# Optimization experiments

Measured on AMD Instinct MI355X. Metric: run time of the kernel, lower is better.

The kernel has to match this reference:

```python
import jax, jax.numpy as jnp
import numpy as np

ATOM_FDIM = 35
BOND_FDIM = 5
MAX_NB = 15
HIDDEN = 512
DEPTH = 6
N_MOLS = 1024
ATOMS_PER_MOL = 32
N_ATOMS = N_MOLS * ATOMS_PER_MOL      # 32768
N_BONDS = 2 * N_ATOMS                  # 65536 (each bond appears in both directions)
N_MESS = 8192                          # tree messages (row 0 is the zero pad slot)
TOTAL_MSG = N_MESS + N_BONDS           # index space for agraph/bgraph


def setup_inputs() -> dict:
    key = jax.random.key(0)
    ks = jax.random.split(key, 8)
    fatoms = jax.random.normal(ks[0], (N_ATOMS, ATOM_FDIM), jnp.float32)
    fbonds = jax.random.normal(ks[1], (N_BONDS, ATOM_FDIM + BOND_FDIM), jnp.float32)
    agraph = jax.random.randint(ks[2], (N_ATOMS, MAX_NB), 0, TOTAL_MSG, dtype=jnp.int32)
    bgraph = jax.random.randint(ks[3], (N_BONDS, MAX_NB), 0, TOTAL_MSG, dtype=jnp.int32)
    # row 0 of the concatenated message table is the padding slot -> zero it
    tree_message = jax.random.normal(ks[4], (N_MESS, HIDDEN), jnp.float32).at[0].set(0.0)
    starts = jnp.arange(N_MOLS, dtype=jnp.int32) * ATOMS_PER_MOL
    scope = jnp.stack([starts, jnp.full((N_MOLS,), ATOMS_PER_MOL, jnp.int32)], axis=1)
    s_i = 1.0 / np.sqrt(ATOM_FDIM + BOND_FDIM)
    s_h = 1.0 / np.sqrt(HIDDEN)
    s_o = 1.0 / np.sqrt(ATOM_FDIM + HIDDEN)
    W_i = jax.random.normal(ks[5], (ATOM_FDIM + BOND_FDIM, HIDDEN), jnp.float32) * s_i
    W_h = jax.random.normal(ks[6], (HIDDEN, HIDDEN), jnp.float32) * s_h
    W_o = jax.random.normal(ks[7], (ATOM_FDIM + HIDDEN, HIDDEN), jnp.float32) * s_o
    b_o = jnp.zeros((HIDDEN,), jnp.float32)
    return {"fatoms": fatoms, "fbonds": fbonds, "agraph": agraph, "bgraph": bgraph,
            "scope": scope, "tree_message": tree_message,
            "W_i": W_i, "W_h": W_h, "W_o": W_o, "b_o": b_o}


def reference(fatoms, fbonds, agraph, bgraph, scope, tree_message, W_i, W_h, W_o, b_o):
    binput = fbonds @ W_i                         # [B, H]
    graph_message = jax.nn.relu(binput)

    def step(gm, _):
        message = jnp.concatenate([tree_message, gm], axis=0)   # [M+B, H]
        nei = message[bgraph].sum(axis=1)                       # gather-sum [B, H]
        return jax.nn.relu(binput + nei @ W_h), None

    graph_message, _ = jax.lax.scan(step, graph_message, None, length=DEPTH - 1)

    message = jnp.concatenate([tree_message, graph_message], axis=0)
    nei = message[agraph].sum(axis=1)             # [A, H]
    ainput = jnp.concatenate([fatoms, nei], axis=1)
    atom_hiddens = jax.nn.relu(ainput @ W_o + b_o)

    # scope is uniform (st = i*ATOMS_PER_MOL, le = ATOMS_PER_MOL) -> static segment ids
    seg = jnp.repeat(jnp.arange(N_MOLS), ATOMS_PER_MOL)
    sums = jax.ops.segment_sum(atom_hiddens, seg, num_segments=N_MOLS)
    return sums / scope[:, 1:].astype(atom_hiddens.dtype)
```

## Files before the change

kernel.cpp:

```cpp
#include <hip/hip_runtime.h>
#include <stdint.h>


#define MAX_NB 15
#define HID 512
#define NA 32768
#define NB 65536
#define NMESS 8192

typedef unsigned short u16;
typedef unsigned int u32;
typedef __bf16 bf16x8 __attribute__((ext_vector_type(8)));
typedef float f32x4 __attribute__((ext_vector_type(4)));

__device__ __forceinline__ u16 f2bf(float f) {
  u32 u = __builtin_bit_cast(u32, f);
  u32 r = (u + 0x7fffu + ((u >> 16) & 1u)) >> 16;
  return (u16)r;
}
__device__ __forceinline__ float bf2f(u16 b) {
  u32 u = ((u32)b) << 16;
  return __builtin_bit_cast(float, u);
}
__device__ __forceinline__ float bflo(u32 u) {
  return __builtin_bit_cast(float, u << 16);
}
__device__ __forceinline__ float bfhi(u32 u) {
  return __builtin_bit_cast(float, u & 0xffff0000u);
}

__device__ __forceinline__ void async16(const u16* g, u16* l) {
  __builtin_amdgcn_global_load_lds(
      (const __attribute__((address_space(1))) u32*)g,
      (__attribute__((address_space(3))) u32*)l, 16, 0, 0);
}

__global__ __launch_bounds__(256) void prep_kernel(
    const float* __restrict__ fbonds, const float* __restrict__ tree,
    const float* __restrict__ Wi, const float* __restrict__ Wh,
    const float* __restrict__ Wo, u16* __restrict__ msg,
    u16* __restrict__ fbpad, u16* __restrict__ wi_t, u16* __restrict__ wh_t,
    u16* __restrict__ wo_t) {
  int t = blockIdx.x * 256 + threadIdx.x;
  const int N0 = NMESS * HID;
  const int N1 = NB * 64;
  const int N2 = 512 * 64;
  const int N3 = 512 * 512;
  const int N4 = 512 * 576;
  if (t < N0) { msg[t] = f2bf(tree[t]); return; }
  t -= N0;
  if (t < N1) {
    int row = t >> 6, c = t & 63;
    fbpad[t] = (c < 40) ? f2bf(fbonds[row * 40 + c]) : (u16)0;
    return;
  }
  t -= N1;
  if (t < N2) {
    int n = t >> 6, k = t & 63;
    wi_t[t] = (k < 40) ? f2bf(Wi[k * 512 + n]) : (u16)0;
    return;
  }
  t -= N2;
  if (t < N3) {
    int n = t >> 9, k = t & 511;
    wh_t[t] = f2bf(Wh[k * 512 + n]);
    return;
  }
  t -= N3;
  if (t < N4) {
    int n = t / 576, k = t - n * 576;
    float v = 0.f;
    if (k < 512) v = Wo[(35 + k) * 512 + n];
    else if (k < 547) v = Wo[(k - 512) * 512 + n];
    wo_t[t] = f2bf(v);
    return;
  }
}

__global__ __launch_bounds__(256) void gather_bonds(
    const u16* __restrict__ msg, const int* __restrict__ bgraph,
    u16* __restrict__ nei) {
  const int xcd = blockIdx.x & 7;
  const int chunk = blockIdx.x >> 3;
  int row = xcd * (NB / 8) + chunk * 4 + (threadIdx.x >> 6);
  int lane = threadIdx.x & 63;
  const int* idxp = bgraph + row * MAX_NB;
  float acc[8] = {0, 0, 0, 0, 0, 0, 0, 0};
#pragma unroll
  for (int j = 0; j < MAX_NB; j++) {
    int id = idxp[j];
    uint4 v = *(const uint4*)(msg + (size_t)id * HID + lane * 8);
    acc[0] += bflo(v.x); acc[1] += bfhi(v.x);
    acc[2] += bflo(v.y); acc[3] += bfhi(v.y);
    acc[4] += bflo(v.z); acc[5] += bfhi(v.z);
    acc[6] += bflo(v.w); acc[7] += bfhi(v.w);
  }
  uint4 o;
  o.x = (u32)f2bf(acc[0]) | ((u32)f2bf(acc[1]) << 16);
  o.y = (u32)f2bf(acc[2]) | ((u32)f2bf(acc[3]) << 16);
  o.z = (u32)f2bf(acc[4]) | ((u32)f2bf(acc[5]) << 16);
  o.w = (u32)f2bf(acc[6]) | ((u32)f2bf(acc[7]) << 16);
  *(uint4*)(nei + (size_t)row * HID + lane * 8) = o;
}

__global__ __launch_bounds__(256) void gather_atoms(
    const u16* __restrict__ msg, const int* __restrict__ agraph,
    const float* __restrict__ fatoms, u16* __restrict__ ainput) {
  const int xcd = blockIdx.x & 7;
  const int chunk = blockIdx.x >> 3;
  int row = xcd * (NA / 8) + chunk * 4 + (threadIdx.x >> 6);
  int lane = threadIdx.x & 63;
  const int* idxp = agraph + row * MAX_NB;
  float acc[8] = {0, 0, 0, 0, 0, 0, 0, 0};
#pragma unroll
  for (int j = 0; j < MAX_NB; j++) {
    int id = idxp[j];
    uint4 v = *(const uint4*)(msg + (size_t)id * HID + lane * 8);
    acc[0] += bflo(v.x); acc[1] += bfhi(v.x);
    acc[2] += bflo(v.y); acc[3] += bfhi(v.y);
    acc[4] += bflo(v.z); acc[5] += bfhi(v.z);
    acc[6] += bflo(v.w); acc[7] += bfhi(v.w);
  }
  uint4 o;
  o.x = (u32)f2bf(acc[0]) | ((u32)f2bf(acc[1]) << 16);
  o.y = (u32)f2bf(acc[2]) | ((u32)f2bf(acc[3]) << 16);
  o.z = (u32)f2bf(acc[4]) | ((u32)f2bf(acc[5]) << 16);
  o.w = (u32)f2bf(acc[6]) | ((u32)f2bf(acc[7]) << 16);
  u16* arow = ainput + (size_t)row * 576;
  *(uint4*)(arow + lane * 8) = o;
  float tv = (lane < 35) ? fatoms[(size_t)row * 35 + lane] : 0.f;
  arow[512 + lane] = f2bf(tv);
}

template <int EPI>
__global__ __launch_bounds__(256) void gemm_k(
    const u16* __restrict__ A, const u16* __restrict__ Bt, int K, int mtx,
    u16* __restrict__ binput, u16* __restrict__ msgout,
    const float* __restrict__ bo, const int* __restrict__ scope,
    float* __restrict__ out) {
  __shared__ __align__(16) u16 As[128 * 32];
  __shared__ __align__(16) u16 Bs[128 * 32];
  const int L = blockIdx.x;
  const int xcd = L & 7;
  const int q = L >> 3;
  const int mBase = (xcd * mtx + (q >> 2)) * 128;
  const int nBase = (q & 3) * 128;
  const int t = threadIdx.x;
  const int lane = t & 63;
  const int w = t >> 6;
  const int wm = w & 1, wn = w >> 1;
  const int r = t >> 2;
  const int c8 = (t & 3) * 8;
  const int q8 = (lane >> 4) * 8;
  const int l15 = lane & 15;

  f32x4 acc[4][4];
#pragma unroll
  for (int i = 0; i < 4; i++)
#pragma unroll
    for (int j = 0; j < 4; j++)
#pragma unroll
      for (int rg = 0; rg < 4; rg++) acc[i][j][rg] = 0.f;

  for (int kb = 0; kb < K; kb += 32) {
    __syncthreads();
    async16(A + (size_t)(mBase + r) * K + kb + c8, As + r * 32 + c8);
    async16(A + (size_t)(mBase + r + 64) * K + kb + c8, As + (r + 64) * 32 + c8);
    async16(Bt + (size_t)(nBase + r) * K + kb + c8, Bs + r * 32 + c8);
    async16(Bt + (size_t)(nBase + r + 64) * K + kb + c8, Bs + (r + 64) * 32 + c8);
    __syncthreads();
    bf16x8 av[4], bv[4];
#pragma unroll
    for (int i = 0; i < 4; i++)
      av[i] = *(const bf16x8*)(As + (wm * 64 + i * 16 + l15) * 32 + q8);
#pragma unroll
    for (int j = 0; j < 4; j++)
      bv[j] = *(const bf16x8*)(Bs + (wn * 64 + j * 16 + l15) * 32 + q8);
#pragma unroll
    for (int i = 0; i < 4; i++)
#pragma unroll
      for (int j = 0; j < 4; j++)
        acc[i][j] = __builtin_amdgcn_mfma_f32_16x16x32_bf16(av[i], bv[j],
                                                            acc[i][j], 0, 0, 0);
  }

  if (EPI == 2) {
#pragma unroll
    for (int m = 0; m < 2; m++) {
      int mol = (mBase + wm * 64 + m * 32) >> 5;
      float inv_le = 1.0f / (float)scope[mol * 2 + 1];
#pragma unroll
      for (int j = 0; j < 4; j++) {
        int col = nBase + wn * 64 + j * 16 + l15;
        float bias = bo[col];
        float s = 0.f;
#pragma unroll
        for (int i = 2 * m; i < 2 * m + 2; i++)
#pragma unroll
          for (int rg = 0; rg < 4; rg++)
            s += fmaxf(acc[i][j][rg] + bias, 0.f);
        s += __shfl_xor(s, 16, 64);
        s += __shfl_xor(s, 32, 64);
        if (lane < 16) out[(size_t)mol * HID + col] = s * inv_le;
      }
    }
  } else {
#pragma unroll
    for (int i = 0; i < 4; i++) {
      int row = mBase + wm * 64 + i * 16 + (lane >> 4) * 4;
#pragma unroll
      for (int j = 0; j < 4; j++) {
        int col = nBase + wn * 64 + j * 16 + l15;
#pragma unroll
        for (int rg = 0; rg < 4; rg++) {
          float v = acc[i][j][rg];
          size_t gi = (size_t)(row + rg) * HID + col;
          if (EPI == 0) {
            binput[gi] = f2bf(v);
            msgout[gi + (size_t)NMESS * HID] = f2bf(fmaxf(v, 0.f));
          } else {
            v += bf2f(binput[gi]);
            msgout[gi + (size_t)NMESS * HID] = f2bf(fmaxf(v, 0.f));
          }
        }
      }
    }
  }
}

extern "C" void kernel_launch(void* const* d_in, const int* in_sizes, int n_in,
                              void* d_out, int out_size, void* d_ws,
                              size_t ws_size, hipStream_t stream) {
  const float* fatoms = (const float*)d_in[0];
  const float* fbonds = (const float*)d_in[1];
  const int* agraph = (const int*)d_in[2];
  const int* bgraph = (const int*)d_in[3];
  const int* scope = (const int*)d_in[4];
  const float* tree = (const float*)d_in[5];
  const float* Wi = (const float*)d_in[6];
  const float* Wh = (const float*)d_in[7];
  const float* Wo = (const float*)d_in[8];
  const float* bo = (const float*)d_in[9];
  float* out = (float*)d_out;

  char* ws = (char*)d_ws;
  u16* msg = (u16*)(ws);
  u16* binput = (u16*)(ws + 75497472ull);
  u16* nei = (u16*)(ws + 142606336ull);
  u16* wi_t = (u16*)(ws + 209715200ull);
  u16* wh_t = (u16*)(ws + 209780736ull);
  u16* wo_t = (u16*)(ws + 210305024ull);
  u16* fbpad = nei;
  u16* ainput = binput;

  prep_kernel<<<35072, 256, 0, stream>>>(fbonds, tree, Wi, Wh, Wo, msg, fbpad,
                                         wi_t, wh_t, wo_t);

  gemm_k<0><<<2048, 256, 0, stream>>>(fbpad, wi_t, 64, 64, binput, msg,
                                      nullptr, nullptr, nullptr);
  for (int d = 0; d < 5; d++) {
    gather_bonds<<<NB / 4, 256, 0, stream>>>(msg, bgraph, nei);
    gemm_k<1><<<2048, 256, 0, stream>>>(nei, wh_t, 512, 64, binput, msg,
                                        nullptr, nullptr, nullptr);
  }
  gather_atoms<<<NA / 4, 256, 0, stream>>>(msg, agraph, fatoms, ainput);
  gemm_k<2><<<1024, 256, 0, stream>>>(ainput, wo_t, 576, 32, nullptr, nullptr,
                                      bo, scope, out);
}
```

Baseline: 1.257 ms.

## Partition gather by column slices per XCD for L2 locality of message table

Restructures the bond and atom gather kernels so each XCD handles two 32-column slices of the hidden dimension across all rows, instead of whole rows for a subset of rows. The intent is that each XCD's L2 only needs to hold its own column slice of the message table. Indices are staged in shared memory with nontemporal loads, and outputs use nontemporal stores. The trade-off is that each gathered load is now only 16 bytes per lane-group (64B per row slice), which reduces coalescing per row and repeats the index fetch for every slice.

Measured after the change: 1.674 ms. +33.1%, slower.

```diff
diff --git a/kernel.cpp b/kernel.cpp
--- a/kernel.cpp
+++ b/kernel.cpp
@@ -12,6 +12,7 @@
 typedef unsigned int u32;
 typedef __bf16 bf16x8 __attribute__((ext_vector_type(8)));
 typedef float f32x4 __attribute__((ext_vector_type(4)));
+typedef u32 u32x4 __attribute__((ext_vector_type(4)));
 
 __device__ __forceinline__ u16 f2bf(float f) {
   u32 u = __builtin_bit_cast(u32, f);
@@ -80,56 +81,105 @@
 __global__ __launch_bounds__(256) void gather_bonds(
     const u16* __restrict__ msg, const int* __restrict__ bgraph,
     u16* __restrict__ nei) {
-  const int xcd = blockIdx.x & 7;
-  const int chunk = blockIdx.x >> 3;
-  int row = xcd * (NB / 8) + chunk * 4 + (threadIdx.x >> 6);
-  int lane = threadIdx.x & 63;
-  const int* idxp = bgraph + row * MAX_NB;
+  __shared__ int sidx[64 * MAX_NB];
+  const int L = blockIdx.x;
+  const int xcd = L & 7;
+  const int q = L >> 3;
+  const int slice = 2 * xcd + (q >> 10);
+  const int chunk = q & 1023;
+  const int t = threadIdx.x;
+
+  const int* gb = bgraph + chunk * (64 * MAX_NB);
+  for (int i = t; i < 64 * MAX_NB; i += 256)
+    sidx[i] = __builtin_nontemporal_load(gb + i);
+  __syncthreads();
+
+  const int lane = t & 63;
+  const int w = t >> 6;
+  const int rl = w * 16 + (lane >> 2);
+  const int sub = lane & 3;
+  const int row = chunk * 64 + rl;
+  const int colOff = slice * 32 + sub * 8;
+
+  int ids[MAX_NB];
+#pragma unroll
+  for (int j = 0; j < MAX_NB; j++) ids[j] = sidx[rl * MAX_NB + j];
+
   float acc[8] = {0, 0, 0, 0, 0, 0, 0, 0};
 #pragma unroll
   for (int j = 0; j < MAX_NB; j++) {
-    int id = idxp[j];
-    uint4 v = *(const uint4*)(msg + (size_t)id * HID + lane * 8);
+    uint4 v = *(const uint4*)(msg + (size_t)ids[j] * HID + colOff);
     acc[0] += bflo(v.x); acc[1] += bfhi(v.x);
     acc[2] += bflo(v.y); acc[3] += bfhi(v.y);
     acc[4] += bflo(v.z); acc[5] += bfhi(v.z);
     acc[6] += bflo(v.w); acc[7] += bfhi(v.w);
   }
-  uint4 o;
+  u32x4 o;
   o.x = (u32)f2bf(acc[0]) | ((u32)f2bf(acc[1]) << 16);
   o.y = (u32)f2bf(acc[2]) | ((u32)f2bf(acc[3]) << 16);
   o.z = (u32)f2bf(acc[4]) | ((u32)f2bf(acc[5]) << 16);
   o.w = (u32)f2bf(acc[6]) | ((u32)f2bf(acc[7]) << 16);
-  *(uint4*)(nei + (size_t)row * HID + lane * 8) = o;
+  __builtin_nontemporal_store(o, (u32x4*)(nei + (size_t)row * HID + colOff));
 }
 
 __global__ __launch_bounds__(256) void gather_atoms(
     const u16* __restrict__ msg, const int* __restrict__ agraph,
     const float* __restrict__ fatoms, u16* __restrict__ ainput) {
-  const int xcd = blockIdx.x & 7;
-  const int chunk = blockIdx.x >> 3;
-  int row = xcd * (NA / 8) + chunk * 4 + (threadIdx.x >> 6);
-  int lane = threadIdx.x & 63;
-  const int* idxp = agraph + row * MAX_NB;
+  __shared__ int sidx[64 * MAX_NB];
+  const int L = blockIdx.x;
+  const int xcd = L & 7;
+  const int q = L >> 3;
+  const int sl = q >> 9;
+  const int slice = 2 * xcd + sl;
+  const int chunk = q & 511;
+  const int t = threadIdx.x;
+
+  const int* ga = agraph + chunk * (64 * MAX_NB);
+  for (int i = t; i < 64 * MAX_NB; i += 256)
+    sidx[i] = __builtin_nontemporal_load(ga + i);
+  __syncthreads();
+
+  const int lane = t & 63;
+  const int w = t >> 6;
+  const int rl = w * 16 + (lane >> 2);
+  const int sub = lane & 3;
+  const int row = chunk * 64 + rl;
+  const int colOff = slice * 32 + sub * 8;
+
+  int ids[MAX_NB];
+#pragma unroll
+  for (int j = 0; j < MAX_NB; j++) ids[j] = sidx[rl * MAX_NB + j];
+
   float acc[8] = {0, 0, 0, 0, 0, 0, 0, 0};
 #pragma unroll
   for (int j = 0; j < MAX_NB; j++) {
-    int id = idxp[j];
-    uint4 v = *(const uint4*)(msg + (size_t)id * HID + lane * 8);
+    uint4 v = *(const uint4*)(msg + (size_t)ids[j] * HID + colOff);
     acc[0] += bflo(v.x); acc[1] += bfhi(v.x);
     acc[2] += bflo(v.y); acc[3] += bfhi(v.y);
     acc[4] += bflo(v.z); acc[5] += bfhi(v.z);
     acc[6] += bflo(v.w); acc[7] += bfhi(v.w);
   }
-  uint4 o;
+  u16* arow = ainput + (size_t)row * 576;
+  u32x4 o;
   o.x = (u32)f2bf(acc[0]) | ((u32)f2bf(acc[1]) << 16);
   o.y = (u32)f2bf(acc[2]) | ((u32)f2bf(acc[3]) << 16);
   o.z = (u32)f2bf(acc[4]) | ((u32)f2bf(acc[5]) << 16);
   o.w = (u32)f2bf(acc[6]) | ((u32)f2bf(acc[7]) << 16);
-  u16* arow = ainput + (size_t)row * 576;
-  *(uint4*)(arow + lane * 8) = o;
-  float tv = (lane < 35) ? fatoms[(size_t)row * 35 + lane] : 0.f;
-  arow[512 + lane] = f2bf(tv);
+  __builtin_nontemporal_store(o, (u32x4*)(arow + colOff));
+
+  if (xcd == 0 && sl == 0) {
+    u32 tw[8];
+#pragma unroll
+    for (int c = 0; c < 8; c++) {
+      int c0 = sub * 16 + 2 * c;
+      float a = (c0 < 35) ? fatoms[(size_t)row * 35 + c0] : 0.f;
+      float b = (c0 + 1 < 35) ? fatoms[(size_t)row * 35 + c0 + 1] : 0.f;
+      tw[c] = (u32)f2bf(a) | ((u32)f2bf(b) << 16);
+    }
+    uint4* tp = (uint4*)(arow + 512 + sub * 16);
+    tp[0] = make_uint4(tw[0], tw[1], tw[2], tw[3]);
+    tp[1] = make_uint4(tw[4], tw[5], tw[6], tw[7]);
+  }
 }
 
 template <int EPI>
@@ -259,11 +309,11 @@
   gemm_k<0><<<2048, 256, 0, stream>>>(fbpad, wi_t, 64, 64, binput, msg,
                                       nullptr, nullptr, nullptr);
   for (int d = 0; d < 5; d++) {
-    gather_bonds<<<NB / 4, 256, 0, stream>>>(msg, bgraph, nei);
+    gather_bonds<<<16384, 256, 0, stream>>>(msg, bgraph, nei);
     gemm_k<1><<<2048, 256, 0, stream>>>(nei, wh_t, 512, 64, binput, msg,
                                         nullptr, nullptr, nullptr);
   }
-  gather_atoms<<<NA / 4, 256, 0, stream>>>(msg, agraph, fatoms, ainput);
+  gather_atoms<<<8192, 256, 0, stream>>>(msg, agraph, fatoms, ainput);
   gemm_k<2><<<1024, 256, 0, stream>>>(ainput, wo_t, 576, 32, nullptr, nullptr,
                                       bo, scope, out);
 }
```

## Fuse neighbor gather-sum into the W_h/W_o GEMMs with ping-pong message buffers

Applied to the files above, without the earlier changes.

Replaces the separate gather kernels and the nei/ainput intermediates with a fused kernel. Each 32-row block gathers the neighbor sums straight into LDS and then multiplies by B, which it reads directly from global memory without staging. The graph messages now alternate between two buffers, and an offset gap lets the gather address the tree table and the current graph buffer as one index space. This removes one global write and read of the 64 MB intermediate per depth step and halves the launch count, but B is re-read from global by every block and the GEMM tile is smaller.

After: 1.513 ms. +20.3%, slower.

```diff
diff --git a/kernel.cpp b/kernel.cpp
--- a/kernel.cpp
+++ b/kernel.cpp
@@ -7,6 +7,7 @@
 #define NA 32768
 #define NB 65536
 #define NMESS 8192
+#define GAPE 33554432u
 
 typedef unsigned short u16;
 typedef unsigned int u32;
@@ -38,7 +39,7 @@
 __global__ __launch_bounds__(256) void prep_kernel(
     const float* __restrict__ fbonds, const float* __restrict__ tree,
     const float* __restrict__ Wi, const float* __restrict__ Wh,
-    const float* __restrict__ Wo, u16* __restrict__ msg,
+    const float* __restrict__ Wo, u16* __restrict__ tab,
     u16* __restrict__ fbpad, u16* __restrict__ wi_t, u16* __restrict__ wh_t,
     u16* __restrict__ wo_t) {
   int t = blockIdx.x * 256 + threadIdx.x;
@@ -47,7 +48,7 @@
   const int N2 = 512 * 64;
   const int N3 = 512 * 512;
   const int N4 = 512 * 576;
-  if (t < N0) { msg[t] = f2bf(tree[t]); return; }
+  if (t < N0) { tab[t] = f2bf(tree[t]); return; }
   t -= N0;
   if (t < N1) {
     int row = t >> 6, c = t & 63;
@@ -77,73 +78,16 @@
   }
 }
 
-__global__ __launch_bounds__(256) void gather_bonds(
-    const u16* __restrict__ msg, const int* __restrict__ bgraph,
-    u16* __restrict__ nei) {
-  const int xcd = blockIdx.x & 7;
-  const int chunk = blockIdx.x >> 3;
-  int row = xcd * (NB / 8) + chunk * 4 + (threadIdx.x >> 6);
-  int lane = threadIdx.x & 63;
-  const int* idxp = bgraph + row * MAX_NB;
-  float acc[8] = {0, 0, 0, 0, 0, 0, 0, 0};
-#pragma unroll
-  for (int j = 0; j < MAX_NB; j++) {
-    int id = idxp[j];
-    uint4 v = *(const uint4*)(msg + (size_t)id * HID + lane * 8);
-    acc[0] += bflo(v.x); acc[1] += bfhi(v.x);
-    acc[2] += bflo(v.y); acc[3] += bfhi(v.y);
-    acc[4] += bflo(v.z); acc[5] += bfhi(v.z);
-    acc[6] += bflo(v.w); acc[7] += bfhi(v.w);
-  }
-  uint4 o;
-  o.x = (u32)f2bf(acc[0]) | ((u32)f2bf(acc[1]) << 16);
-  o.y = (u32)f2bf(acc[2]) | ((u32)f2bf(acc[3]) << 16);
-  o.z = (u32)f2bf(acc[4]) | ((u32)f2bf(acc[5]) << 16);
-  o.w = (u32)f2bf(acc[6]) | ((u32)f2bf(acc[7]) << 16);
-  *(uint4*)(nei + (size_t)row * HID + lane * 8) = o;
-}
-
-__global__ __launch_bounds__(256) void gather_atoms(
-    const u16* __restrict__ msg, const int* __restrict__ agraph,
-    const float* __restrict__ fatoms, u16* __restrict__ ainput) {
-  const int xcd = blockIdx.x & 7;
-  const int chunk = blockIdx.x >> 3;
-  int row = xcd * (NA / 8) + chunk * 4 + (threadIdx.x >> 6);
-  int lane = threadIdx.x & 63;
-  const int* idxp = agraph + row * MAX_NB;
-  float acc[8] = {0, 0, 0, 0, 0, 0, 0, 0};
-#pragma unroll
-  for (int j = 0; j < MAX_NB; j++) {
-    int id = idxp[j];
-    uint4 v = *(const uint4*)(msg + (size_t)id * HID + lane * 8);
-    acc[0] += bflo(v.x); acc[1] += bfhi(v.x);
-    acc[2] += bflo(v.y); acc[3] += bfhi(v.y);
-    acc[4] += bflo(v.z); acc[5] += bfhi(v.z);
-    acc[6] += bflo(v.w); acc[7] += bfhi(v.w);
-  }
-  uint4 o;
-  o.x = (u32)f2bf(acc[0]) | ((u32)f2bf(acc[1]) << 16);
-  o.y = (u32)f2bf(acc[2]) | ((u32)f2bf(acc[3]) << 16);
-  o.z = (u32)f2bf(acc[4]) | ((u32)f2bf(acc[5]) << 16);
-  o.w = (u32)f2bf(acc[6]) | ((u32)f2bf(acc[7]) << 16);
-  u16* arow = ainput + (size_t)row * 576;
-  *(uint4*)(arow + lane * 8) = o;
-  float tv = (lane < 35) ? fatoms[(size_t)row * 35 + lane] : 0.f;
-  arow[512 + lane] = f2bf(tv);
-}
-
-template <int EPI>
-__global__ __launch_bounds__(256) void gemm_k(
-    const u16* __restrict__ A, const u16* __restrict__ Bt, int K, int mtx,
-    u16* __restrict__ binput, u16* __restrict__ msgout,
-    const float* __restrict__ bo, const int* __restrict__ scope,
-    float* __restrict__ out) {
+__global__ __launch_bounds__(256) void gemm_init(
+    const u16* __restrict__ A, const u16* __restrict__ Bt,
+    u16* __restrict__ binput, u16* __restrict__ graphA) {
+  const int K = 64;
   __shared__ __align__(16) u16 As[128 * 32];
   __shared__ __align__(16) u16 Bs[128 * 32];
   const int L = blockIdx.x;
   const int xcd = L & 7;
   const int q = L >> 3;
-  const int mBase = (xcd * mtx + (q >> 2)) * 128;
+  const int mBase = (xcd * 64 + (q >> 2)) * 128;
   const int nBase = (q & 3) * 128;
   const int t = threadIdx.x;
   const int lane = t & 63;
@@ -184,44 +128,136 @@
                                                             acc[i][j], 0, 0, 0);
   }
 
-  if (EPI == 2) {
-#pragma unroll
-    for (int m = 0; m < 2; m++) {
-      int mol = (mBase + wm * 64 + m * 32) >> 5;
-      float inv_le = 1.0f / (float)scope[mol * 2 + 1];
-#pragma unroll
-      for (int j = 0; j < 4; j++) {
-        int col = nBase + wn * 64 + j * 16 + l15;
-        float bias = bo[col];
-        float s = 0.f;
-#pragma unroll
-        for (int i = 2 * m; i < 2 * m + 2; i++)
-#pragma unroll
-          for (int rg = 0; rg < 4; rg++)
-            s += fmaxf(acc[i][j][rg] + bias, 0.f);
-        s += __shfl_xor(s, 16, 64);
-        s += __shfl_xor(s, 32, 64);
-        if (lane < 16) out[(size_t)mol * HID + col] = s * inv_le;
+#pragma unroll
+  for (int i = 0; i < 4; i++) {
+    int row = mBase + wm * 64 + i * 16 + (lane >> 4) * 4;
+#pragma unroll
+    for (int j = 0; j < 4; j++) {
+      int col = nBase + wn * 64 + j * 16 + l15;
+#pragma unroll
+      for (int rg = 0; rg < 4; rg++) {
+        float v = acc[i][j][rg];
+        size_t gi = (size_t)(row + rg) * HID + col;
+        binput[gi] = f2bf(v);
+        graphA[gi] = f2bf(fmaxf(v, 0.f));
       }
     }
+  }
+}
+
+template <int ATOMS>
+__global__ __launch_bounds__(256, 3) void fused_gg(
+    const u16* __restrict__ tab, const int* __restrict__ graph,
+    const u16* __restrict__ Bt, const u16* __restrict__ binput,
+    const float* __restrict__ fatoms, const float* __restrict__ bo,
+    const int* __restrict__ scope, u16* __restrict__ outGraph,
+    float* __restrict__ out, u32 gap) {
+  constexpr int K = ATOMS ? 576 : 512;
+  constexpr int NT = K / 32;
+  __shared__ __align__(16) u16 As[NT * 1024];
+  __shared__ int sidx[32 * MAX_NB];
+  const int mBase = blockIdx.x * 32;
+  const int t = threadIdx.x;
+  for (int i = t; i < 32 * MAX_NB; i += 256)
+    sidx[i] = graph[mBase * MAX_NB + i];
+  __syncthreads();
+
+  const int lane = t & 63;
+  const int w = t >> 6;
+  for (int r = 0; r < 8; r++) {
+    const int rl = w * 8 + r;
+    float acc[8] = {0, 0, 0, 0, 0, 0, 0, 0};
+#pragma unroll
+    for (int j = 0; j < MAX_NB; j++) {
+      int id = sidx[rl * MAX_NB + j];
+      u32 off = (u32)id * HID + (id >= NMESS ? gap : 0u);
+      uint4 v = *(const uint4*)(tab + off + lane * 8);
+      acc[0] += bflo(v.x); acc[1] += bfhi(v.x);
+      acc[2] += bflo(v.y); acc[3] += bfhi(v.y);
+      acc[4] += bflo(v.z); acc[5] += bfhi(v.z);
+      acc[6] += bflo(v.w); acc[7] += bfhi(v.w);
+    }
+    uint4 o;
+    o.x = (u32)f2bf(acc[0]) | ((u32)f2bf(acc[1]) << 16);
+    o.y = (u32)f2bf(acc[2]) | ((u32)f2bf(acc[3]) << 16);
+    o.z = (u32)f2bf(acc[4]) | ((u32)f2bf(acc[5]) << 16);
+    o.w = (u32)f2bf(acc[6]) | ((u32)f2bf(acc[7]) << 16);
+    *(uint4*)(As + (lane >> 2) * 1024 + rl * 32 + (lane & 3) * 8) = o;
+    if (ATOMS) {
+      if (lane < 8) {
+        u32 tw[4];
+#pragma unroll
+        for (int c = 0; c < 4; c++) {
+          int c0 = lane * 8 + 2 * c;
+          float a = (c0 < 35) ? fatoms[(size_t)(mBase + rl) * 35 + c0] : 0.f;
+          float b =
+              (c0 + 1 < 35) ? fatoms[(size_t)(mBase + rl) * 35 + c0 + 1] : 0.f;
+          tw[c] = (u32)f2bf(a) | ((u32)f2bf(b) << 16);
+        }
+        *(uint4*)(As + (16 + (lane >> 2)) * 1024 + rl * 32 + (lane & 3) * 8) =
+            make_uint4(tw[0], tw[1], tw[2], tw[3]);
+      }
+    }
+  }
+  __syncthreads();
+
+  const int l15 = lane & 15;
+  const int q8 = (lane >> 4) * 8;
+  const int nq = w;
+  f32x4 acc2[2][8];
+#pragma unroll
+  for (int i = 0; i < 2; i++)
+#pragma unroll
+    for (int j = 0; j < 8; j++)
+#pragma unroll
+      for (int rg = 0; rg < 4; rg++) acc2[i][j][rg] = 0.f;
+
+  for (int kbi = 0; kbi < NT; kbi++) {
+    bf16x8 av0 = *(const bf16x8*)(As + kbi * 1024 + l15 * 32 + q8);
+    bf16x8 av1 = *(const bf16x8*)(As + kbi * 1024 + (16 + l15) * 32 + q8);
+    bf16x8 bv[8];
+#pragma unroll
+    for (int j = 0; j < 8; j++)
+      bv[j] = *(const bf16x8*)(Bt + (size_t)(nq * 128 + j * 16 + l15) * K +
+                               kbi * 32 + q8);
+#pragma unroll
+    for (int j = 0; j < 8; j++) {
+      acc2[0][j] =
+          __builtin_amdgcn_mfma_f32_16x16x32_bf16(av0, bv[j], acc2[0][j], 0, 0, 0);
+      acc2[1][j] =
+          __builtin_amdgcn_mfma_f32_16x16x32_bf16(av1, bv[j], acc2[1][j], 0, 0, 0);
+    }
+  }
+
+  if (ATOMS) {
+    const int mol = blockIdx.x;
+    float inv = 1.0f / (float)scope[mol * 2 + 1];
+#pragma unroll
+    for (int j = 0; j < 8; j++) {
+      int col = nq * 128 + j * 16 + l15;
+      float bias = bo[col];
+      float s = 0.f;
+#pragma unroll
+      for (int i = 0; i < 2; i++)
+#pragma unroll
+        for (int rg = 0; rg < 4; rg++)
+          s += fmaxf(acc2[i][j][rg] + bias, 0.f);
+      s += __shfl_xor(s, 16, 64);
+      s += __shfl_xor(s, 32, 64);
+      if (lane < 16) out[(size_t)mol * HID + col] = s * inv;
+    }
   } else {
 #pragma unroll
-    for (int i = 0; i < 4; i++) {
-      int row = mBase + wm * 64 + i * 16 + (lane >> 4) * 4;
-#pragma unroll
-      for (int j = 0; j < 4; j++) {
-        int col = nBase + wn * 64 + j * 16 + l15;
+    for (int i = 0; i < 2; i++) {
+      int row = mBase + i * 16 + (lane >> 4) * 4;
+#pragma unroll
+      for (int j = 0; j < 8; j++) {
+        int col = nq * 128 + j * 16 + l15;
 #pragma unroll
         for (int rg = 0; rg < 4; rg++) {
-          float v = acc[i][j][rg];
           size_t gi = (size_t)(row + rg) * HID + col;
-          if (EPI == 0) {
-            binput[gi] = f2bf(v);
-            msgout[gi + (size_t)NMESS * HID] = f2bf(fmaxf(v, 0.f));
-          } else {
-            v += bf2f(binput[gi]);
-            msgout[gi + (size_t)NMESS * HID] = f2bf(fmaxf(v, 0.f));
-          }
+          float v = acc2[i][j][rg] + bf2f(binput[gi]);
+          outGraph[gi] = f2bf(fmaxf(v, 0.f));
         }
       }
     }
@@ -243,27 +279,27 @@
   const float* bo = (const float*)d_in[9];
   float* out = (float*)d_out;
 
-  char* ws = (char*)d_ws;
-  u16* msg = (u16*)(ws);
-  u16* binput = (u16*)(ws + 75497472ull);
-  u16* nei = (u16*)(ws + 142606336ull);
-  u16* wi_t = (u16*)(ws + 209715200ull);
-  u16* wh_t = (u16*)(ws + 209780736ull);
-  u16* wo_t = (u16*)(ws + 210305024ull);
-  u16* fbpad = nei;
-  u16* ainput = binput;
-
-  prep_kernel<<<35072, 256, 0, stream>>>(fbonds, tree, Wi, Wh, Wo, msg, fbpad,
+  u16* tab = (u16*)d_ws;
+  u16* graphA = tab + (size_t)NMESS * HID;
+  u16* graphB = graphA + (size_t)NB * HID;
+  u16* binput = graphB + (size_t)NB * HID;
+  u16* wi_t = binput + (size_t)NB * HID;
+  u16* wh_t = wi_t + 512 * 64;
+  u16* wo_t = wh_t + 512 * 512;
+  u16* fbpad = graphB;
+
+  prep_kernel<<<35072, 256, 0, stream>>>(fbonds, tree, Wi, Wh, Wo, tab, fbpad,
                                          wi_t, wh_t, wo_t);
 
-  gemm_k<0><<<2048, 256, 0, stream>>>(fbpad, wi_t, 64, 64, binput, msg,
-                                      nullptr, nullptr, nullptr);
+  gemm_init<<<2048, 256, 0, stream>>>(fbpad, wi_t, binput, graphA);
+
+  const u32 gaps[5] = {0u, GAPE, 0u, GAPE, 0u};
+  u16* const outs[5] = {graphB, graphA, graphB, graphA, graphB};
   for (int d = 0; d < 5; d++) {
-    gather_bonds<<<NB / 4, 256, 0, stream>>>(msg, bgraph, nei);
-    gemm_k<1><<<2048, 256, 0, stream>>>(nei, wh_t, 512, 64, binput, msg,
-                                        nullptr, nullptr, nullptr);
-  }
-  gather_atoms<<<NA / 4, 256, 0, stream>>>(msg, agraph, fatoms, ainput);
-  gemm_k<2><<<1024, 256, 0, stream>>>(ainput, wo_t, 576, 32, nullptr, nullptr,
-                                      bo, scope, out);
-}
+    fused_gg<0><<<2048, 256, 0, stream>>>(tab, bgraph, wh_t, binput, nullptr,
+                                          nullptr, nullptr, outs[d], nullptr,
+                                          gaps[d]);
+  }
+  fused_gg<1><<<1024, 256, 0, stream>>>(tab, agraph, wo_t, nullptr, fatoms, bo,
+                                        scope, nullptr, out, GAPE);
+}
```

## Recompute bond input inside depth GEMM by concatenating W_i and W_h along K

Applied to the files above, without the earlier changes.

Instead of storing binput (fbonds@W_i) and reloading it in every depth-step epilogue, each depth GEMM now runs over a concatenated K dimension: the padded fbonds (64 cols) followed by the gathered neighbor sum (512 cols), against a stacked W_i/W_h weight matrix. This removes the binput write and the five bf16 binput reads of a 65536x512 matrix, and it also avoids rounding binput to bf16. In exchange each depth GEMM does about 12% more MFMA work and the K loop picks its source pointer per iteration.

Result: no change. 1.243 ms (-1.1%).

```diff
diff --git a/kernel.cpp b/kernel.cpp
--- a/kernel.cpp
+++ b/kernel.cpp
@@ -18,10 +18,6 @@
   u32 r = (u + 0x7fffu + ((u >> 16) & 1u)) >> 16;
   return (u16)r;
 }
-__device__ __forceinline__ float bf2f(u16 b) {
-  u32 u = ((u32)b) << 16;
-  return __builtin_bit_cast(float, u);
-}
 __device__ __forceinline__ float bflo(u32 u) {
   return __builtin_bit_cast(float, u << 16);
 }
@@ -39,14 +35,12 @@
     const float* __restrict__ fbonds, const float* __restrict__ tree,
     const float* __restrict__ Wi, const float* __restrict__ Wh,
     const float* __restrict__ Wo, u16* __restrict__ msg,
-    u16* __restrict__ fbpad, u16* __restrict__ wi_t, u16* __restrict__ wh_t,
-    u16* __restrict__ wo_t) {
+    u16* __restrict__ fbpad, u16* __restrict__ wcat, u16* __restrict__ wo_t) {
   int t = blockIdx.x * 256 + threadIdx.x;
   const int N0 = NMESS * HID;
   const int N1 = NB * 64;
-  const int N2 = 512 * 64;
-  const int N3 = 512 * 512;
-  const int N4 = 512 * 576;
+  const int N2 = 512 * 576;
+  const int N3 = 512 * 576;
   if (t < N0) { msg[t] = f2bf(tree[t]); return; }
   t -= N0;
   if (t < N1) {
@@ -56,18 +50,15 @@
   }
   t -= N1;
   if (t < N2) {
-    int n = t >> 6, k = t & 63;
-    wi_t[t] = (k < 40) ? f2bf(Wi[k * 512 + n]) : (u16)0;
+    int n = t / 576, k = t - n * 576;
+    float v = 0.f;
+    if (k < 40) v = Wi[k * 512 + n];
+    else if (k >= 64) v = Wh[(k - 64) * 512 + n];
+    wcat[t] = f2bf(v);
     return;
   }
   t -= N2;
   if (t < N3) {
-    int n = t >> 9, k = t & 511;
-    wh_t[t] = f2bf(Wh[k * 512 + n]);
-    return;
-  }
-  t -= N3;
-  if (t < N4) {
     int n = t / 576, k = t - n * 576;
     float v = 0.f;
     if (k < 512) v = Wo[(35 + k) * 512 + n];
@@ -134,10 +125,10 @@
 
 template <int EPI>
 __global__ __launch_bounds__(256) void gemm_k(
-    const u16* __restrict__ A, const u16* __restrict__ Bt, int K, int mtx,
-    u16* __restrict__ binput, u16* __restrict__ msgout,
-    const float* __restrict__ bo, const int* __restrict__ scope,
-    float* __restrict__ out) {
+    const u16* __restrict__ A1, int s1, int kSplit,
+    const u16* __restrict__ A2, const u16* __restrict__ Bt, int Bstride, int K,
+    int mtx, u16* __restrict__ msgout, const float* __restrict__ bo,
+    const int* __restrict__ scope, float* __restrict__ out) {
   __shared__ __align__(16) u16 As[128 * 32];
   __shared__ __align__(16) u16 Bs[128 * 32];
   const int L = blockIdx.x;
@@ -163,11 +154,17 @@
       for (int rg = 0; rg < 4; rg++) acc[i][j][rg] = 0.f;
 
   for (int kb = 0; kb < K; kb += 32) {
+    const u16* Ab;
+    int Astr, kOff;
+    if (kb < kSplit) { Ab = A1; Astr = s1; kOff = kb; }
+    else { Ab = A2; Astr = 512; kOff = kb - kSplit; }
     __syncthreads();
-    async16(A + (size_t)(mBase + r) * K + kb + c8, As + r * 32 + c8);
-    async16(A + (size_t)(mBase + r + 64) * K + kb + c8, As + (r + 64) * 32 + c8);
-    async16(Bt + (size_t)(nBase + r) * K + kb + c8, Bs + r * 32 + c8);
-    async16(Bt + (size_t)(nBase + r + 64) * K + kb + c8, Bs + (r + 64) * 32 + c8);
+    async16(Ab + (size_t)(mBase + r) * Astr + kOff + c8, As + r * 32 + c8);
+    async16(Ab + (size_t)(mBase + r + 64) * Astr + kOff + c8,
+            As + (r + 64) * 32 + c8);
+    async16(Bt + (size_t)(nBase + r) * Bstride + kb + c8, Bs + r * 32 + c8);
+    async16(Bt + (size_t)(nBase + r + 64) * Bstride + kb + c8,
+            Bs + (r + 64) * 32 + c8);
     __syncthreads();
     bf16x8 av[4], bv[4];
 #pragma unroll
@@ -213,15 +210,8 @@
         int col = nBase + wn * 64 + j * 16 + l15;
 #pragma unroll
         for (int rg = 0; rg < 4; rg++) {
-          float v = acc[i][j][rg];
           size_t gi = (size_t)(row + rg) * HID + col;
-          if (EPI == 0) {
-            binput[gi] = f2bf(v);
-            msgout[gi + (size_t)NMESS * HID] = f2bf(fmaxf(v, 0.f));
-          } else {
-            v += bf2f(binput[gi]);
-            msgout[gi + (size_t)NMESS * HID] = f2bf(fmaxf(v, 0.f));
-          }
+          msgout[(size_t)NMESS * HID + gi] = f2bf(fmaxf(acc[i][j][rg], 0.f));
         }
       }
     }
@@ -245,25 +235,23 @@
 
   char* ws = (char*)d_ws;
   u16* msg = (u16*)(ws);
-  u16* binput = (u16*)(ws + 75497472ull);
-  u16* nei = (u16*)(ws + 142606336ull);
-  u16* wi_t = (u16*)(ws + 209715200ull);
-  u16* wh_t = (u16*)(ws + 209780736ull);
-  u16* wo_t = (u16*)(ws + 210305024ull);
-  u16* fbpad = nei;
-  u16* ainput = binput;
+  u16* nei = (u16*)(ws + 75497472ull);
+  u16* fbpad = (u16*)(ws + 142606336ull);
+  u16* wcat = (u16*)(ws + 150994944ull);
+  u16* wo_t = (u16*)(ws + 151584768ull);
+  u16* ainput = nei;
 
   prep_kernel<<<35072, 256, 0, stream>>>(fbonds, tree, Wi, Wh, Wo, msg, fbpad,
-                                         wi_t, wh_t, wo_t);
-
-  gemm_k<0><<<2048, 256, 0, stream>>>(fbpad, wi_t, 64, 64, binput, msg,
-                                      nullptr, nullptr, nullptr);
+                                         wcat, wo_t);
+
+  gemm_k<0><<<2048, 256, 0, stream>>>(fbpad, 64, 64, nullptr, wcat, 576, 64,
+                                      64, msg, nullptr, nullptr, nullptr);
   for (int d = 0; d < 5; d++) {
     gather_bonds<<<NB / 4, 256, 0, stream>>>(msg, bgraph, nei);
-    gemm_k<1><<<2048, 256, 0, stream>>>(nei, wh_t, 512, 64, binput, msg,
-                                        nullptr, nullptr, nullptr);
+    gemm_k<0><<<2048, 256, 0, stream>>>(fbpad, 64, 64, nei, wcat, 576, 576,
+                                        64, msg, nullptr, nullptr, nullptr);
   }
   gather_atoms<<<NA / 4, 256, 0, stream>>>(msg, agraph, fatoms, ainput);
-  gemm_k<2><<<1024, 256, 0, stream>>>(ainput, wo_t, 576, 32, nullptr, nullptr,
-                                      bo, scope, out);
-}
+  gemm_k<2><<<1024, 256, 0, stream>>>(ainput, 576, 576, nullptr, wo_t, 576,
+                                      576, 32, nullptr, bo, scope, out);
+}
```
